# Kernel optimization log

Measured on AMD Instinct MI355X. Metric: run time of the kernel, lower is better.

Reference implementation:

```python
import jax, jax.numpy as jnp
import numpy as np

N_EMBD = 1024
N_HEAD = 16

def setup_inputs() -> dict:
    key = jax.random.key(0)
    ks = jax.random.split(key, 5)
    B, T, C = 4, 2048, N_EMBD
    s = 0.02
    return {
        'x': jax.random.normal(ks[0], (B, T, C), jnp.float32),
        'w_attn': jax.random.normal(ks[1], (C, 3 * C), jnp.float32) * s,
        'b_attn': jax.random.normal(ks[2], (3 * C,), jnp.float32) * s,
        'w_proj': jax.random.normal(ks[3], (C, C), jnp.float32) * s,
        'b_proj': jax.random.normal(ks[4], (C,), jnp.float32) * s,
    }

def reference(x, w_attn, b_attn, w_proj, b_proj):
    B, T, C = x.shape
    H = N_HEAD
    D = C // H  # head dim
    qkv = x @ w_attn + b_attn                      # [B,T,3C]
    q, k, v = jnp.split(qkv, 3, axis=-1)
    q = q.reshape(B, T, H, D).transpose(0, 2, 1, 3)  # [B,H,T,D]
    k = k.reshape(B, T, H, D).transpose(0, 2, 1, 3)
    v = v.reshape(B, T, H, D).transpose(0, 2, 1, 3)
    att = jnp.einsum('bhqd,bhkd->bhqk', q, k) * (1.0 / jnp.sqrt(jnp.float32(D)))
    causal = jnp.tril(jnp.ones((T, T), bool))
    att = jnp.where(causal[None, None], att, jnp.float32(-jnp.inf))
    att = jax.nn.softmax(att, axis=-1)
    y = jnp.einsum('bhqk,bhkd->bhqd', att, v)      # [B,H,T,D]
    y = y.transpose(0, 2, 1, 3).reshape(B, T, C)
    return y @ w_proj + b_proj
```

## Files before the change

### kernel.cpp

```cpp
#include <hip/hip_runtime.h>
#include <math.h>

typedef short s16x8 __attribute__((ext_vector_type(8)));
typedef unsigned short u16;
typedef unsigned short u16x4 __attribute__((ext_vector_type(4)));
typedef float f32x4 __attribute__((ext_vector_type(4)));

__device__ __forceinline__ f32x4 mfma16(s16x8 a, s16x8 b, f32x4 c) {
  return __builtin_amdgcn_mfma_f32_16x16x32_bf16(a, b, c, 0, 0, 0);
}

__device__ __forceinline__ u16 f2bf(float f) {
  unsigned u = __builtin_bit_cast(unsigned, f);
  u = (u + 0x7fffu + ((u >> 16) & 1u)) >> 16;
  return (u16)u;
}

__device__ __forceinline__ unsigned pk_trunc(float hi, float lo) {
  return __builtin_amdgcn_perm(__builtin_bit_cast(unsigned, hi),
                               __builtin_bit_cast(unsigned, lo), 0x07060302u);
}

__device__ __forceinline__ s16x8 mk_pa(unsigned a, unsigned b, unsigned c, unsigned d) {
  union { unsigned u[4]; s16x8 h; } t;
  t.u[0] = a; t.u[1] = b; t.u[2] = c; t.u[3] = d;
  return t.h;
}

__device__ __forceinline__ void gll16(const void* g, void* l) {
  __builtin_amdgcn_global_load_lds((__attribute__((address_space(1))) void*)(void*)g,
                                   (__attribute__((address_space(3))) void*)l,
                                   16, 0, 0);
}

__device__ __forceinline__ void transpose_body(const float* __restrict__ in,
                                               u16* __restrict__ out, int R, int C,
                                               int bx, int by, float (*tile)[33]) {
  int c0 = bx * 32, r0 = by * 32;
  int tx = threadIdx.x & 31, ty = threadIdx.x >> 5;
#pragma unroll
  for (int s = 0; s < 4; ++s)
    tile[ty + 8 * s][tx] = in[(size_t)(r0 + ty + 8 * s) * C + c0 + tx];
  __syncthreads();
#pragma unroll
  for (int s = 0; s < 4; ++s)
    out[(size_t)(c0 + ty + 8 * s) * R + r0 + tx] = f2bf(tile[tx][ty + 8 * s]);
}

__global__ __launch_bounds__(256) void k_prep(const float* __restrict__ x,
                                              u16* __restrict__ xb,
                                              const float* __restrict__ w_attn,
                                              u16* __restrict__ waT,
                                              const float* __restrict__ w_proj,
                                              u16* __restrict__ wpT) {
  __shared__ float tile[32][33];
  int id = blockIdx.x;
  if (id < 4096) {
    int i = (id * 256 + threadIdx.x) * 8;
    const float4* xv = (const float4*)(x + i);
    float4 a = xv[0], b = xv[1];
    union { s16x8 v; u16 s[8]; } r;
    r.s[0] = f2bf(a.x); r.s[1] = f2bf(a.y); r.s[2] = f2bf(a.z); r.s[3] = f2bf(a.w);
    r.s[4] = f2bf(b.x); r.s[5] = f2bf(b.y); r.s[6] = f2bf(b.z); r.s[7] = f2bf(b.w);
    *(s16x8*)(xb + i) = r.v;
  } else if (id < 4096 + 3072) {
    int t = id - 4096;
    transpose_body(w_attn, waT, 1024, 3072, t % 96, t / 96, tile);
  } else {
    int t = id - (4096 + 3072);
    transpose_body(w_proj, wpT, 1024, 1024, t % 32, t / 32, tile);
  }
}

template <int EPI>
__global__ __launch_bounds__(256) void k_gemm(const u16* __restrict__ A,
                                              const u16* __restrict__ Bt,
                                              const float* __restrict__ bias,
                                              float* __restrict__ outp,
                                              u16* __restrict__ q_out,
                                              u16* __restrict__ k_out,
                                              u16* __restrict__ vt_out,
                                              int K, int nIter) {
  __shared__ u16 As[2][4096];
  __shared__ u16 Bs[2][4096];
  int tid = threadIdx.x, w = tid >> 6, l = tid & 63;
  int r = l & 15, qd = l >> 4;
  int id = blockIdx.x;
  int xcd = id & 7, s0 = id >> 3;
  int mBlk = xcd * 8 + (s0 & 7);
  int nBlk = s0 >> 3;
  f32x4 acc[4][4] = {};

  const u16* ga[2]; const u16* gb[2]; int lgrp[2];
#pragma unroll
  for (int qq = 0; qq < 2; ++qq) {
    int grp = 2 * w + qq;
    int rowA = mBlk * 128 + grp * 16 + (l >> 2);
    int rowB = nBlk * 128 + grp * 16 + (l >> 2);
    int kcol = (l & 3) * 8;
    ga[qq] = A + (size_t)rowA * K + kcol;
    gb[qq] = Bt + (size_t)rowB * K + kcol;
    lgrp[qq] = grp * 512;
  }
  int aoff = ((w & 1) * 4) * 512 + r * 32 + qd * 8;
  int boff = ((w >> 1) * 4) * 512 + r * 32 + qd * 8;

  auto stageg = [&](int kt, int buf) {
#pragma unroll
    for (int qq = 0; qq < 2; ++qq) {
      gll16(ga[qq] + kt * 32, As[buf] + lgrp[qq]);
      gll16(gb[qq] + kt * 32, Bs[buf] + lgrp[qq]);
    }
  };

  stageg(0, 0);
  __syncthreads();

  for (int kt = 0; kt < nIter; ++kt) {
    int cur = kt & 1;
    if (kt + 1 < nIter) stageg(kt + 1, cur ^ 1);
    s16x8 af[4], bf[4];
#pragma unroll
    for (int i = 0; i < 4; ++i) af[i] = *(const s16x8*)(As[cur] + aoff + i * 512);
#pragma unroll
    for (int j = 0; j < 4; ++j) bf[j] = *(const s16x8*)(Bs[cur] + boff + j * 512);
#pragma unroll
    for (int i = 0; i < 4; ++i)
#pragma unroll
      for (int j = 0; j < 4; ++j) acc[i][j] = mfma16(af[i], bf[j], acc[i][j]);
    __syncthreads();
  }

  const float QSCALE = 0.125f * 1.44269504088896f;
  int rowBase = mBlk * 128 + (w & 1) * 64;
  int colBase = nBlk * 128 + (w >> 1) * 64;
#pragma unroll
  for (int i = 0; i < 4; ++i) {
#pragma unroll
    for (int j = 0; j < 4; ++j) {
      int col = colBase + j * 16 + r;
      float bv = bias[col];
      float vv[4];
#pragma unroll
      for (int g = 0; g < 4; ++g) vv[g] = acc[i][j][g] + bv;
      int row0 = rowBase + i * 16 + qd * 4;
      if (EPI == 0) {
        int which = col >> 10;
        int rem = col & 1023;
        int hh = rem >> 6, dd = rem & 63;
        int bb = row0 >> 11, tt0 = row0 & 2047;
        if (which == 2) {
          u16x4 pk;
#pragma unroll
          for (int g = 0; g < 4; ++g) pk[g] = f2bf(vv[g]);
          *(u16x4*)(vt_out + (((size_t)(bb * 16 + hh)) * 64 + dd) * 2048 + tt0) = pk;
        } else {
          u16* base = (which == 0) ? q_out : k_out;
#pragma unroll
          for (int g = 0; g < 4; ++g) {
            float v = vv[g];
            if (which == 0) v *= QSCALE;
            base[(((size_t)(bb * 16 + hh)) * 2048 + tt0 + g) * 64 + dd] = f2bf(v);
          }
        }
      } else {
#pragma unroll
        for (int g = 0; g < 4; ++g)
          outp[(size_t)(row0 + g) * 1024 + col] = vv[g];
      }
    }
  }
}

__global__ __launch_bounds__(256) void k_gemmP(const u16* __restrict__ A,
                                               const u16* __restrict__ Bt,
                                               const float* __restrict__ bias,
                                               float* __restrict__ outp) {
  __shared__ u16 As[2][128 * 32];
  __shared__ u16 Bs[2][64 * 32];
  const int K = 1024;
  int tid = threadIdx.x, w = tid >> 6, l = tid & 63;
  int r = l & 15, qd = l >> 4;
  int wm = w >> 1, wn = w & 1;
  int id = blockIdx.x;
  int xcd = id & 7, s0 = id >> 3;
  int mBlk = xcd * 8 + (s0 & 7);
  int nBlk = s0 >> 3;
  f32x4 acc[4][2] = {};

  int kcol = (tid & 3) * 8;
  const u16* ga = A + (size_t)(mBlk * 128 + (tid >> 2)) * K + kcol;
  const u16* gb = Bt + (size_t)(nBlk * 64 + (tid >> 2)) * K + kcol;
  int aoff = (wm * 64 + r) * 32 + qd * 8;
  int boff = (wn * 32 + r) * 32 + qd * 8;

  auto stageg = [&](int kt, int buf) {
    gll16(ga + kt * 32, (char*)As[buf] + w * 1024);
    gll16(ga + (size_t)64 * K + kt * 32, (char*)As[buf] + 4096 + w * 1024);
    gll16(gb + kt * 32, (char*)Bs[buf] + w * 1024);
  };

  stageg(0, 0);
  __syncthreads();

  for (int kt = 0; kt < 32; ++kt) {
    int cur = kt & 1;
    if (kt + 1 < 32) stageg(kt + 1, cur ^ 1);
    s16x8 af[4], bf[2];
#pragma unroll
    for (int i = 0; i < 4; ++i) af[i] = *(const s16x8*)(As[cur] + aoff + i * 512);
#pragma unroll
    for (int j = 0; j < 2; ++j) bf[j] = *(const s16x8*)(Bs[cur] + boff + j * 512);
#pragma unroll
    for (int i = 0; i < 4; ++i)
#pragma unroll
      for (int j = 0; j < 2; ++j) acc[i][j] = mfma16(af[i], bf[j], acc[i][j]);
    __syncthreads();
  }

  int rowBase = mBlk * 128 + wm * 64;
  int colBase = nBlk * 64 + wn * 32;
#pragma unroll
  for (int i = 0; i < 4; ++i) {
#pragma unroll
    for (int j = 0; j < 2; ++j) {
      int col = colBase + j * 16 + r;
      float bv = bias[col];
      int row0 = rowBase + i * 16 + qd * 4;
#pragma unroll
      for (int g = 0; g < 4; ++g)
        outp[(size_t)(row0 + g) * 1024 + col] = acc[i][j][g] + bv;
    }
  }
}

__global__ __launch_bounds__(256, 4) void k_attn(const u16* __restrict__ qg,
                                                 const u16* __restrict__ kg,
                                                 const u16* __restrict__ vtg,
                                                 u16* __restrict__ yg) {
  __shared__ u16 Ks[2][64 * 64];
  __shared__ u16 Vs[2][64 * 64];

  int id = blockIdx.x;
  int xcd = id & 7;
  int slot = id >> 3;
  int bx = 4 * (slot >> 5) + (slot & 3);
  int bh = (((slot >> 2) & 7) << 3) | xcd;
  int bb = bh >> 4, hh = bh & 15;
  int tid = threadIdx.x, w = tid >> 6, l = tid & 63;
  int r = l & 15, qd = l >> 4;

  const int chunk0 = bx, chunk1 = 31 - bx;
  int nmax = 32 - bx;
  int qloc = w * 16 + r;

  s16x8 qf[2][2];
#pragma unroll
  for (int c = 0; c < 2; ++c) {
    int qbase = (c ? chunk1 : chunk0) * 64 + w * 16;
#pragma unroll
    for (int s = 0; s < 2; ++s)
      qf[c][s] = *(const s16x8*)(qg + ((size_t)bh * 2048 + qbase + r) * 64 + s * 32 + qd * 8);
  }

  f32x4 o[2][4] = {};
  float lsum[2] = {0.f, 0.f};

  int rl = l >> 3;
  int cg = (l & 7) ^ rl;
  const u16* kbase = kg + (size_t)bh * 2048 * 64;
  const u16* vbase = vtg + (size_t)bh * 64 * 2048;

  auto stage = [&](int kt, int buf) {
    int kk0 = kt * 64;
#pragma unroll
    for (int p = 0; p < 2; ++p) {
      int row = p * 32 + w * 8 + rl;
      gll16(kbase + ((size_t)(kk0 + row)) * 64 + cg * 8, Ks[buf] + p * 2048 + w * 512);
      gll16(vbase + (size_t)row * 2048 + kk0 + cg * 8, Vs[buf] + p * 2048 + w * 512);
    }
  };

  auto smax = [&](f32x4 (&sc)[4], s16x8 (&pac)[2], bool mask, float& sum) {
    unsigned pk[4][2];
#pragma unroll
    for (int j = 0; j < 4; ++j) {
      float p0, p1, p2, p3;
      if (mask) {
        int kb0 = 16 * j + 4 * qd;
        p0 = (kb0 + 0 > qloc) ? 0.f : __builtin_amdgcn_exp2f(sc[j][0]);
        p1 = (kb0 + 1 > qloc) ? 0.f : __builtin_amdgcn_exp2f(sc[j][1]);
        p2 = (kb0 + 2 > qloc) ? 0.f : __builtin_amdgcn_exp2f(sc[j][2]);
        p3 = (kb0 + 3 > qloc) ? 0.f : __builtin_amdgcn_exp2f(sc[j][3]);
      } else {
        p0 = __builtin_amdgcn_exp2f(sc[j][0]);
        p1 = __builtin_amdgcn_exp2f(sc[j][1]);
        p2 = __builtin_amdgcn_exp2f(sc[j][2]);
        p3 = __builtin_amdgcn_exp2f(sc[j][3]);
      }
      sum += (p0 + p1) + (p2 + p3);
      pk[j][0] = pk_trunc(p1, p0);
      pk[j][1] = pk_trunc(p3, p2);
    }
#pragma unroll
    for (int s = 0; s < 2; ++s) {
      unsigned a0 = pk[2 * s][0], b0 = pk[2 * s + 1][0];
      asm("v_permlane32_swap_b32 %0, %1" : "+v"(a0), "+v"(b0));
      asm("v_permlane16_swap_b32 %0, %1" : "+v"(a0), "+v"(b0));
      unsigned a1 = pk[2 * s][1], b1 = pk[2 * s + 1][1];
      asm("v_permlane32_swap_b32 %0, %1" : "+v"(a1), "+v"(b1));
      asm("v_permlane16_swap_b32 %0, %1" : "+v"(a1), "+v"(b1));
      pac[s] = mk_pa(a0, a1, b0, b1);
    }
  };

  stage(0, 0);
  __syncthreads();

  for (int kt = 0; kt < nmax; ++kt) {
    int cur = kt & 1;
    if (kt + 1 < nmax) stage(kt + 1, cur ^ 1);
    bool act0 = (kt <= bx);

    f32x4 s0[4], s1[4];
#pragma unroll
    for (int j = 0; j < 4; ++j) {
      s1[j] = f32x4{0.f, 0.f, 0.f, 0.f};
      if (act0) s0[j] = f32x4{0.f, 0.f, 0.f, 0.f};
    }
    __builtin_amdgcn_s_setprio(1);
#pragma unroll
    for (int s = 0; s < 2; ++s) {
#pragma unroll
      for (int j = 0; j < 4; ++j) {
        s16x8 kf = *(const s16x8*)(Ks[cur] + (16 * j + r) * 64 + ((s * 4 + qd) ^ (r & 7)) * 8);
        s1[j] = mfma16(kf, qf[1][s], s1[j]);
        if (act0) s0[j] = mfma16(kf, qf[0][s], s0[j]);
      }
    }
    __builtin_amdgcn_s_setprio(0);

    s16x8 pa0[2], pa1[2];
    smax(s1, pa1, kt == chunk1, lsum[1]);
    if (act0) smax(s0, pa0, kt == chunk0, lsum[0]);

    __builtin_amdgcn_s_setprio(1);
#pragma unroll
    for (int s = 0; s < 2; ++s) {
#pragma unroll
      for (int j = 0; j < 4; ++j) {
        s16x8 vf = *(const s16x8*)(Vs[cur] + (16 * j + r) * 64 + ((s * 4 + qd) ^ (r & 7)) * 8);
        o[1][j] = mfma16(vf, pa1[s], o[1][j]);
        if (act0) o[0][j] = mfma16(vf, pa0[s], o[0][j]);
      }
    }
    __builtin_amdgcn_s_setprio(0);

    __syncthreads();
  }

#pragma unroll
  for (int c = 0; c < 2; ++c) {
    int qbase = (c ? chunk1 : chunk0) * 64 + w * 16;
    float tot = lsum[c];
    tot += __shfl_xor(tot, 16);
    tot += __shfl_xor(tot, 32);
    float inv = 1.0f / tot;
    size_t rowoff = ((size_t)bb * 2048 + qbase + r) * 1024 + hh * 64;
#pragma unroll
    for (int j = 0; j < 4; ++j) {
      u16x4 yv;
      yv[0] = f2bf(o[c][j][0] * inv);
      yv[1] = f2bf(o[c][j][1] * inv);
      yv[2] = f2bf(o[c][j][2] * inv);
      yv[3] = f2bf(o[c][j][3] * inv);
      *(u16x4*)(yg + rowoff + 16 * j + 4 * qd) = yv;
    }
  }
}

extern "C" void kernel_launch(void* const* d_in, const int* in_sizes, int n_in,
                              void* d_out, int out_size, void* d_ws, size_t ws_size,
                              hipStream_t stream) {
  const float* x      = (const float*)d_in[0];
  const float* w_attn = (const float*)d_in[1];
  const float* b_attn = (const float*)d_in[2];
  const float* w_proj = (const float*)d_in[3];
  const float* b_proj = (const float*)d_in[4];
  float* out = (float*)d_out;

  char* ws = (char*)d_ws;
  size_t off = 0;
  auto alloc = [&](size_t bytes) -> void* {
    void* p = ws + off;
    off += (bytes + 255) & ~(size_t)255;
    return p;
  };
  const size_t BT = 8192, C = 1024;
  u16* xb  = (u16*)alloc(BT * C * 2);
  u16* waT = (u16*)alloc(3072 * 1024 * 2);
  u16* wpT = (u16*)alloc(1024 * 1024 * 2);
  u16* qb  = (u16*)alloc(BT * C * 2);
  u16* kb  = (u16*)alloc(BT * C * 2);
  u16* vtb = (u16*)alloc(BT * C * 2);
  (void)ws_size; (void)in_sizes; (void)n_in; (void)out_size;

  k_prep<<<4096 + 3072 + 1024, 256, 0, stream>>>(x, xb, w_attn, waT, w_proj, wpT);
  k_gemm<0><<<1536, 256, 0, stream>>>(xb, waT, b_attn, nullptr, qb, kb, vtb, 1024, 32);
  k_attn<<<1024, 256, 0, stream>>>(qb, kb, vtb, xb );
  k_gemmP<<<1024, 256, 0, stream>>>(xb, wpT, b_proj, out);
}
```

Baseline: 237.7 us.

## Software-pipeline attention loop with triple-buffered K/V and QK lookahead

Switches the K/V shared-memory staging from double to triple buffering, with loads issued two tiles ahead. The loop is restructured so the QK^T MFMAs and softmax for tile kt+1 sit next to the PV MFMAs for tile kt, letting matrix and exp/permute work interleave. The cost is more LDS and registers, and launch bounds drop from 4 to 3 blocks per SM, which may reduce occupancy.

```diff
diff --git a/kernel.cpp b/kernel.cpp
--- a/kernel.cpp
+++ b/kernel.cpp
@@ -234,12 +234,12 @@
   }
 }
 
-__global__ __launch_bounds__(256, 4) void k_attn(const u16* __restrict__ qg,
+__global__ __launch_bounds__(256, 3) void k_attn(const u16* __restrict__ qg,
                                                  const u16* __restrict__ kg,
                                                  const u16* __restrict__ vtg,
                                                  u16* __restrict__ yg) {
-  __shared__ u16 Ks[2][64 * 64];
-  __shared__ u16 Vs[2][64 * 64];
+  __shared__ u16 Ks[3][64 * 64];
+  __shared__ u16 Vs[3][64 * 64];
 
   int id = blockIdx.x;
   int xcd = id & 7;
@@ -279,6 +279,39 @@
       gll16(kbase + ((size_t)(kk0 + row)) * 64 + cg * 8, Ks[buf] + p * 2048 + w * 512);
       gll16(vbase + (size_t)row * 2048 + kk0 + cg * 8, Vs[buf] + p * 2048 + w * 512);
     }
+  };
+
+  auto qk = [&](int buf, f32x4 (&sc0)[4], f32x4 (&sc1)[4], bool act0) {
+#pragma unroll
+    for (int j = 0; j < 4; ++j) {
+      sc1[j] = f32x4{0.f, 0.f, 0.f, 0.f};
+      if (act0) sc0[j] = f32x4{0.f, 0.f, 0.f, 0.f};
+    }
+    __builtin_amdgcn_s_setprio(1);
+#pragma unroll
+    for (int s = 0; s < 2; ++s) {
+#pragma unroll
+      for (int j = 0; j < 4; ++j) {
+        s16x8 kf = *(const s16x8*)(Ks[buf] + (16 * j + r) * 64 + ((s * 4 + qd) ^ (r & 7)) * 8);
+        sc1[j] = mfma16(kf, qf[1][s], sc1[j]);
+        if (act0) sc0[j] = mfma16(kf, qf[0][s], sc0[j]);
+      }
+    }
+    __builtin_amdgcn_s_setprio(0);
+  };
+
+  auto pv = [&](int buf, s16x8 (&pa0)[2], s16x8 (&pa1)[2], bool act0) {
+    __builtin_amdgcn_s_setprio(1);
+#pragma unroll
+    for (int s = 0; s < 2; ++s) {
+#pragma unroll
+      for (int j = 0; j < 4; ++j) {
+        s16x8 vf = *(const s16x8*)(Vs[buf] + (16 * j + r) * 64 + ((s * 4 + qd) ^ (r & 7)) * 8);
+        o[1][j] = mfma16(vf, pa1[s], o[1][j]);
+        if (act0) o[0][j] = mfma16(vf, pa0[s], o[0][j]);
+      }
+    }
+    __builtin_amdgcn_s_setprio(0);
   };
 
   auto smax = [&](f32x4 (&sc)[4], s16x8 (&pac)[2], bool mask, float& sum) {
@@ -315,48 +348,38 @@
   };
 
   stage(0, 0);
+  stage(1, 1);
   __syncthreads();
 
+  f32x4 cs0[4], cs1[4];
+  qk(0, cs0, cs1, true);
+  s16x8 pa0c[2], pa1c[2];
+  smax(cs1, pa1c, 0 == chunk1, lsum[1]);
+  smax(cs0, pa0c, 0 == chunk0, lsum[0]);
+
+  int b0 = 0, b1 = 1, b2 = 2;
   for (int kt = 0; kt < nmax; ++kt) {
-    int cur = kt & 1;
-    if (kt + 1 < nmax) stage(kt + 1, cur ^ 1);
-    bool act0 = (kt <= bx);
-
-    f32x4 s0[4], s1[4];
-#pragma unroll
-    for (int j = 0; j < 4; ++j) {
-      s1[j] = f32x4{0.f, 0.f, 0.f, 0.f};
-      if (act0) s0[j] = f32x4{0.f, 0.f, 0.f, 0.f};
-    }
-    __builtin_amdgcn_s_setprio(1);
-#pragma unroll
-    for (int s = 0; s < 2; ++s) {
-#pragma unroll
-      for (int j = 0; j < 4; ++j) {
-        s16x8 kf = *(const s16x8*)(Ks[cur] + (16 * j + r) * 64 + ((s * 4 + qd) ^ (r & 7)) * 8);
-        s1[j] = mfma16(kf, qf[1][s], s1[j]);
-        if (act0) s0[j] = mfma16(kf, qf[0][s], s0[j]);
-      }
-    }
-    __builtin_amdgcn_s_setprio(0);
-
-    s16x8 pa0[2], pa1[2];
-    smax(s1, pa1, kt == chunk1, lsum[1]);
-    if (act0) smax(s0, pa0, kt == chunk0, lsum[0]);
-
-    __builtin_amdgcn_s_setprio(1);
-#pragma unroll
-    for (int s = 0; s < 2; ++s) {
-#pragma unroll
-      for (int j = 0; j < 4; ++j) {
-        s16x8 vf = *(const s16x8*)(Vs[cur] + (16 * j + r) * 64 + ((s * 4 + qd) ^ (r & 7)) * 8);
-        o[1][j] = mfma16(vf, pa1[s], o[1][j]);
-        if (act0) o[0][j] = mfma16(vf, pa0[s], o[0][j]);
-      }
-    }
-    __builtin_amdgcn_s_setprio(0);
+    if (kt + 2 < nmax) stage(kt + 2, b2);
+    bool act0c = (kt <= bx);
+    bool haven = (kt + 1 < nmax);
+    bool act0n = (kt + 1 <= bx);
+
+    f32x4 ns0[4], ns1[4];
+    if (haven) qk(b1, ns0, ns1, act0n);
+    pv(b0, pa0c, pa1c, act0c);
+
+    s16x8 pa0n[2], pa1n[2];
+    if (haven) {
+      smax(ns1, pa1n, (kt + 1) == chunk1, lsum[1]);
+      if (act0n) smax(ns0, pa0n, (kt + 1) == chunk0, lsum[0]);
+    }
 
     __syncthreads();
+    int t = b0; b0 = b1; b1 = b2; b2 = t;
+    if (haven) {
+      pa1c[0] = pa1n[0]; pa1c[1] = pa1n[1];
+      if (act0n) { pa0c[0] = pa0n[0]; pa0c[1] = pa0n[1]; }
+    }
   }
 
 #pragma unroll
```

Measured after the change: 253.4 us. +6.6%, slower.
